# Optimization experiments

Hardware: AMD Instinct MI355X
Metric: run time of the kernel (lower is better)

## Reference

```python
import jax, jax.numpy as jnp
import numpy as np

SINK_MAX = 128  # max materialized sink tokens (atten_sink counts are < 64)
NEG_INF = -1e30


def _gather_paged(kv, block_table, pos):
    """Gather tokens from a paged KV cache.
    kv: [num_blocks, block_size, 2, Hkv, D]; block_table: [B, max_blocks] int;
    pos: [B, L] token positions (assumed clipped to valid range).
    Returns [B, L, 2, Hkv, D]."""
    nb, bs = kv.shape[0], kv.shape[1]
    B = pos.shape[0]
    blk = jnp.take_along_axis(block_table, pos // bs, axis=1)  # [B, L]
    flat_idx = blk * bs + pos % bs                              # [B, L]
    kv_flat = kv.reshape(nb * bs, *kv.shape[2:])
    return kv_flat[flat_idx]


def setup_inputs() -> dict:
    key = jax.random.key(0)
    ks = jax.random.split(key, 6)
    B, H, Hkv, D = 32, 32, 4, 128
    NB, BS, NBC = 2048, 128, 512
    MAX_BLK, MAX_CBLK, NSEL = 64, 16, 256
    query = jax.random.normal(ks[0], (B, H, D), dtype=jnp.float32)
    ori_kv = jax.random.normal(ks[1], (NB, BS, 2, Hkv, D), dtype=jnp.float32)
    cmp_kv = jax.random.normal(ks[2], (NBC, BS, 2, Hkv, D), dtype=jnp.float32)
    ori_block_table = (jnp.arange(B * MAX_BLK) % NB).reshape(B, MAX_BLK).astype(jnp.int32)
    cmp_block_table = (jnp.arange(B * MAX_CBLK) % NBC).reshape(B, MAX_CBLK).astype(jnp.int32)
    atten_sink = jax.random.randint(ks[3], (B,), 1, 64, dtype=jnp.int32)
    seqused_kv = jax.random.randint(ks[4], (B,), 4096, 8192, dtype=jnp.int32)
    cmp_sparse_indices = jnp.sort(jax.random.randint(ks[5], (B, NSEL), 0, 1024, dtype=jnp.int32), axis=1)
    return {
        'query_npu': query,
        'q_act_seqs_npu': jnp.ones((B,), dtype=jnp.int32),
        'ori_kv_npu': ori_kv,
        'cmp_kv_npu': cmp_kv,
        'ori_block_table_npu': ori_block_table,
        'cmp_block_table_npu': cmp_block_table,
        'atten_sink_npu': atten_sink,
        'seqused_kv_npu': seqused_kv,
        'cmp_sparse_indices_npu': cmp_sparse_indices,
        'softmax_scale': float(1.0 / np.sqrt(D)),
        'win_size': 512,
        'cmp_ratio': 4,
    }


def reference(query_npu, q_act_seqs_npu, ori_kv_npu, cmp_kv_npu,
              ori_block_table_npu, cmp_block_table_npu, atten_sink_npu,
              seqused_kv_npu, cmp_sparse_indices_npu, softmax_scale,
              win_size, cmp_ratio):
    B, H, D = query_npu.shape
    Hkv = ori_kv_npu.shape[3]
    G = H // Hkv
    bs = ori_kv_npu.shape[1]
    seq = seqused_kv_npu[:, None].astype(jnp.int32)          # [B,1]
    sink = atten_sink_npu[:, None].astype(jnp.int32)         # [B,1]

    # --- sink tokens (first atten_sink tokens of the original cache) ---
    pos_s = jnp.broadcast_to(jnp.arange(SINK_MAX, dtype=jnp.int32)[None, :], (B, SINK_MAX))
    mask_s = (pos_s < sink) & (pos_s < seq)
    kv_s = _gather_paged(ori_kv_npu, ori_block_table_npu, jnp.clip(pos_s, 0))

    # --- sliding window (last win_size original tokens, excluding sink overlap) ---
    pos_w = seq - win_size + jnp.arange(win_size, dtype=jnp.int32)[None, :]
    mask_w = (pos_w >= 0) & (pos_w >= sink)
    kv_w = _gather_paged(ori_kv_npu, ori_block_table_npu, jnp.clip(pos_w, 0))

    # --- sparse-selected compressed tokens ---
    cmp_len = seq // cmp_ratio
    idx_c = cmp_sparse_indices_npu.astype(jnp.int32)         # [B, NSEL]
    mask_c = idx_c < cmp_len
    kv_c = _gather_paged(cmp_kv_npu, cmp_block_table_npu, jnp.clip(idx_c, 0))

    # --- combine all KV sources: [B, L, 2, Hkv, D] ---
    kv = jnp.concatenate([kv_s, kv_w, kv_c], axis=1)
    k, v = kv[:, :, 0], kv[:, :, 1]                           # [B, L, Hkv, D]
    mask = jnp.concatenate([mask_s, mask_w, mask_c], axis=1)  # [B, L]

    # --- GQA attention: heads grouped per kv head ---
    q = query_npu.reshape(B, Hkv, G, D)
    logits = jnp.einsum('bkgd,blkd->bkgl', q, k) * softmax_scale
    logits = jnp.where(mask[:, None, None, :], logits, NEG_INF)
    p = jax.nn.softmax(logits, axis=-1)
    out = jnp.einsum('bkgl,blkd->bkgd', p, v)
    return out.reshape(B, H, D)
```

## Files before the change

kernel.cpp:

```cpp
#include <hip/hip_runtime.h>

constexpr int B_    = 32;
constexpr int H_    = 32;
constexpr int HKV_  = 4;
constexpr int G_    = 8;
constexpr int D_    = 128;
constexpr int BS_   = 128;
constexpr int MAXBLK_  = 64;
constexpr int MAXCBLK_ = 16;
constexpr int NSEL_    = 256;
constexpr int SINKMAX_ = 128;
constexpr int WIN_     = 512;
constexpr int P_       = 8;
constexpr float MSHIFT = 24.0f;

__global__ __launch_bounds__(256, 4) void sfa_partial_kernel(
    const float* __restrict__ q,
    const float* __restrict__ ori_kv,
    const float* __restrict__ cmp_kv,
    const int*   __restrict__ ori_bt,
    const int*   __restrict__ cmp_bt,
    const int*   __restrict__ sinkp,
    const int*   __restrict__ seqp,
    const int*   __restrict__ selp,
    const float* __restrict__ scalep,
    const int*   __restrict__ ratiop,
    float* __restrict__ o_out,
    float* __restrict__ s_out)
{
  const int part = blockIdx.x;
  const int kh   = blockIdx.y;
  const int b    = blockIdx.z;
  const int tid  = threadIdx.x;
  const int grp  = tid >> 5;
  const int j    = tid & 31;
  const int wave = tid >> 6;
  const int h    = ((j & 1) << 2) | (j & 2) | ((j >> 2) & 1);

  const float scale = scalep[0];
  const int ratio   = ratiop[0];
  const int seq     = seqp[b];
  const int sink    = sinkp[b];
  const int cmp_len = seq / ratio;

  const int sbt0 = ori_bt[b * MAXBLK_];
  int wbase = seq - WIN_; if (wbase < 0) wbase = 0;
  const int w0 = wbase >> 7;
  auto obt = [&](int k) { int w = w0 + k; if (w > MAXBLK_ - 1) w = MAXBLK_ - 1;
                          return ori_bt[b * MAXBLK_ + w]; };
  const int wb0 = obt(0), wb1 = obt(1), wb2 = obt(2), wb3 = obt(3), wb4 = obt(4);
  const int cb0 = cmp_bt[b * MAXCBLK_ + 0], cb1 = cmp_bt[b * MAXCBLK_ + 1];
  const int cb2 = cmp_bt[b * MAXCBLK_ + 2], cb3 = cmp_bt[b * MAXCBLK_ + 3];
  const int cb4 = cmp_bt[b * MAXCBLK_ + 4], cb5 = cmp_bt[b * MAXCBLK_ + 5];
  const int cb6 = cmp_bt[b * MAXCBLK_ + 6], cb7 = cmp_bt[b * MAXCBLK_ + 7];

  float4 qf[G_];
  const float* qb = q + ((size_t)b * H_ + (size_t)kh * G_) * D_ + 4 * j;
#pragma unroll
  for (int g = 0; g < G_; ++g) qf[g] = *(const float4*)(qb + g * D_);

  float  s_acc = 0.f;
  float4 oacc[G_];
#pragma unroll
  for (int m = 0; m < G_; ++m) oacc[m] = make_float4(0.f, 0.f, 0.f, 0.f);

  int s_end = sink; if (s_end < 0) s_end = 0; if (s_end > SINKMAX_) s_end = SINKMAX_;
  const int sB0 = s_end;
  const int sC0 = s_end + WIN_;
  const int L   = s_end + WIN_ + NSEL_;
  const int chunk = (L + P_ - 1) / P_;
  const int lo = part * chunk;
  int hi = lo + chunk; if (hi > L) hi = L;

  auto process = [&](const float4 kf, const float4 vf, const float msk) {
    float lg[G_];
#pragma unroll
    for (int g = 0; g < G_; ++g)
      lg[g] = qf[g].x * kf.x + qf[g].y * kf.y + qf[g].z * kf.z + qf[g].w * kf.w;
    const bool p0 = j & 1, p1 = j & 2, p2 = j & 4;
    float s4[4];
#pragma unroll
    for (int i4 = 0; i4 < 4; ++i4) {
      const float keep = p0 ? lg[4 + i4] : lg[i4];
      const float send = p0 ? lg[i4]     : lg[4 + i4];
      s4[i4] = keep + __shfl_xor(send, 1, 64);
    }
    float s2[2];
#pragma unroll
    for (int i2 = 0; i2 < 2; ++i2) {
      const float keep = p1 ? s4[2 + i2] : s4[i2];
      const float send = p1 ? s4[i2]     : s4[2 + i2];
      s2[i2] = keep + __shfl_xor(send, 2, 64);
    }
    const float keep = p2 ? s2[1] : s2[0];
    const float send = p2 ? s2[0] : s2[1];
    float v1 = keep + __shfl_xor(send, 4, 64);
    v1 += __shfl_xor(v1, 8, 64);
    v1 += __shfl_xor(v1, 16, 64);
    const float e = __expf(fminf(fmaf(v1, scale, -MSHIFT), 80.f)) * msk;
    s_acc += e;
    const float g2a = e,   g2b = __shfl_xor(e, 4, 64);
    const float g4a = g2a, g4b = g2b;
    const float g4c = __shfl_xor(g2a, 2, 64), g4d = __shfl_xor(g2b, 2, 64);
    const float pm0 = g4a, pm1 = g4b, pm2 = g4c, pm3 = g4d;
    const float pm4 = __shfl_xor(g4a, 1, 64), pm5 = __shfl_xor(g4b, 1, 64);
    const float pm6 = __shfl_xor(g4c, 1, 64), pm7 = __shfl_xor(g4d, 1, 64);
    oacc[0].x += pm0 * vf.x; oacc[0].y += pm0 * vf.y; oacc[0].z += pm0 * vf.z; oacc[0].w += pm0 * vf.w;
    oacc[1].x += pm1 * vf.x; oacc[1].y += pm1 * vf.y; oacc[1].z += pm1 * vf.z; oacc[1].w += pm1 * vf.w;
    oacc[2].x += pm2 * vf.x; oacc[2].y += pm2 * vf.y; oacc[2].z += pm2 * vf.z; oacc[2].w += pm2 * vf.w;
    oacc[3].x += pm3 * vf.x; oacc[3].y += pm3 * vf.y; oacc[3].z += pm3 * vf.z; oacc[3].w += pm3 * vf.w;
    oacc[4].x += pm4 * vf.x; oacc[4].y += pm4 * vf.y; oacc[4].z += pm4 * vf.z; oacc[4].w += pm4 * vf.w;
    oacc[5].x += pm5 * vf.x; oacc[5].y += pm5 * vf.y; oacc[5].z += pm5 * vf.z; oacc[5].w += pm5 * vf.w;
    oacc[6].x += pm6 * vf.x; oacc[6].y += pm6 * vf.y; oacc[6].z += pm6 * vf.z; oacc[6].w += pm6 * vf.w;
    oacc[7].x += pm7 * vf.x; oacc[7].y += pm7 * vf.y; oacc[7].z += pm7 * vf.z; oacc[7].w += pm7 * vf.w;
  };

#define SEG_LOOP(S0X, S1X, ADDR_CODE)                                          \
  {                                                                            \
    const int s0q = (S0X), s1q = (S1X);                                        \
    int iq = s0q + ((lo + grp - s0q) & 7);                                     \
    if (iq < s1q) {                                                            \
      const float* kbC; float mC;                                              \
      { const int ti = iq; const float* akb; float amsk; ADDR_CODE;            \
        kbC = akb; mC = amsk; }                                                \
      float4 kfC = *(const float4*)(kbC + 4 * j);                              \
      float4 vfC = *(const float4*)(kbC + HKV_ * D_ + 4 * j);                  \
      for (; iq < s1q; iq += 8) {                                              \
        int inq = iq + 8; if (inq >= s1q) inq = s1q - 1;                       \
        const float* kbN; float mN;                                            \
        { const int ti = inq; const float* akb; float amsk; ADDR_CODE;         \
          kbN = akb; mN = amsk; }                                              \
        const float4 kfN = *(const float4*)(kbN + 4 * j);                      \
        const float4 vfN = *(const float4*)(kbN + HKV_ * D_ + 4 * j);          \
        process(kfC, vfC, mC);                                                 \
        kfC = kfN; vfC = vfN; mC = mN;                                         \
      }                                                                        \
    }                                                                          \
  }

  SEG_LOOP(lo, (hi < sB0 ? hi : sB0), {
    amsk = (ti < seq) ? 1.f : 0.f;
    akb = ori_kv + (((size_t)(sbt0 * BS_ + ti)) << 10) + kh * D_;
  });

  SEG_LOOP((lo > sB0 ? lo : sB0), (hi < sC0 ? hi : sC0), {
    const int pos = seq - WIN_ + (ti - sB0);
    amsk = (pos >= 0 && pos >= sink) ? 1.f : 0.f;
    const int pc = pos > 0 ? pos : 0;
    const int wi = (pc >> 7) - w0;
    int blk = wb0;
    blk = (wi == 1) ? wb1 : blk; blk = (wi == 2) ? wb2 : blk;
    blk = (wi == 3) ? wb3 : blk; blk = (wi == 4) ? wb4 : blk;
    akb = ori_kv + (((size_t)(blk * BS_ + (pc & (BS_ - 1)))) << 10) + kh * D_;
  });

  SEG_LOOP((lo > sC0 ? lo : sC0), hi, {
    const int idx = selp[b * NSEL_ + (ti - sC0)];
    amsk = (idx < cmp_len) ? 1.f : 0.f;
    const int pc = idx > 0 ? idx : 0;
    const int ci = pc >> 7;
    int blk = cb0;
    blk = (ci == 1) ? cb1 : blk; blk = (ci == 2) ? cb2 : blk;
    blk = (ci == 3) ? cb3 : blk; blk = (ci == 4) ? cb4 : blk;
    blk = (ci == 5) ? cb5 : blk; blk = (ci == 6) ? cb6 : blk;
    blk = (ci == 7) ? cb7 : blk;
    akb = cmp_kv + (((size_t)(blk * BS_ + (pc & (BS_ - 1)))) << 10) + kh * D_;
  });
#undef SEG_LOOP

  s_acc += __shfl_xor(s_acc, 32, 64);
  float* of = reinterpret_cast<float*>(oacc);
#pragma unroll
  for (int t = 0; t < 32; ++t) of[t] += __shfl_xor(of[t], 32, 64);

  __shared__ float lds_o[4][G_][D_];
  __shared__ float lds_s[4][G_];
  if ((tid & 63) < 32) {
#pragma unroll
    for (int m = 0; m < G_; ++m)
      *(float4*)&lds_o[wave][h ^ m][4 * j] = oacc[m];
    if (j < 8) lds_s[wave][h] = s_acc;
  }
  __syncthreads();

#pragma unroll
  for (int e = tid; e < G_ * D_; e += 256) {
    const int g = e >> 7, d = e & (D_ - 1);
    const float num = lds_o[0][g][d] + lds_o[1][g][d] + lds_o[2][g][d] + lds_o[3][g][d];
    o_out[(((size_t)(b * HKV_ + kh) * P_ + part) * G_ + g) * D_ + d] = num;
  }
  if (tid < G_) {
    s_out[((size_t)(b * HKV_ + kh) * P_ + part) * G_ + tid] =
        lds_s[0][tid] + lds_s[1][tid] + lds_s[2][tid] + lds_s[3][tid];
  }
}

__global__ __launch_bounds__(256) void sfa_combine_kernel(
    const float* __restrict__ op, const float* __restrict__ sp,
    float* __restrict__ out)
{
  const int idx = blockIdx.x * 256 + threadIdx.x;
  const int d  = idx & (D_ - 1);
  const int hh = (idx >> 7) & (H_ - 1);
  const int b  = idx >> 12;
  const int kh = hh >> 3, g = hh & 7;
  float num = 0.f, den = 0.f;
#pragma unroll
  for (int p = 0; p < P_; ++p) {
    num += op[(((size_t)(b * HKV_ + kh) * P_ + p) * G_ + g) * D_ + d];
    den += sp[((size_t)(b * HKV_ + kh) * P_ + p) * G_ + g];
  }
  out[idx] = num / den;
}

extern "C" void kernel_launch(void* const* d_in, const int* in_sizes, int n_in,
                              void* d_out, int out_size, void* d_ws, size_t ws_size,
                              hipStream_t stream) {
  const float* q      = (const float*)d_in[0];
  const float* ori_kv = (const float*)d_in[2];
  const float* cmp_kv = (const float*)d_in[3];
  const int*   ori_bt = (const int*)d_in[4];
  const int*   cmp_bt = (const int*)d_in[5];
  const int*   sinkp  = (const int*)d_in[6];
  const int*   seqp   = (const int*)d_in[7];
  const int*   selp   = (const int*)d_in[8];
  const float* scalep = (const float*)d_in[9];
  const int*   ratiop = (const int*)d_in[11];
  float* out = (float*)d_out;

  float* op = (float*)d_ws;
  float* sp = op + (size_t)P_ * B_ * HKV_ * G_ * D_;

  sfa_partial_kernel<<<dim3(P_, HKV_, B_), 256, 0, stream>>>(
      q, ori_kv, cmp_kv, ori_bt, cmp_bt, sinkp, seqp, selp, scalep, ratiop,
      op, sp);
  sfa_combine_kernel<<<(B_ * H_ * D_) / 256, 256, 0, stream>>>(op, sp, out);
}
```

Measured before the change: 27.63 us.

## Stream KV rows into LDS with async global_load_lds and a 4-deep pipeline

Replaces the three per-segment register-prefetch loops with one unified loop over the partition. K/V rows are issued through global_load_lds into a per-wave 4-stage LDS ring, with manual vmcnt waits. Masks are precomputed into a bitmask, and the selected indices are preloaded into lanes and fetched by shuffle. The aim is more memory requests in flight to hide gather latency, at the cost of branchy unified address math, LDS round trips, and reliance on exact vmcnt accounting.

Result: slower. 72.02 us (+160.6%).

```diff
diff --git a/kernel.cpp b/kernel.cpp
--- a/kernel.cpp
+++ b/kernel.cpp
@@ -1,4 +1,5 @@
 #include <hip/hip_runtime.h>
+#include <stdint.h>
 
 constexpr int B_    = 32;
 constexpr int H_    = 32;
@@ -12,7 +13,14 @@
 constexpr int SINKMAX_ = 128;
 constexpr int WIN_     = 512;
 constexpr int P_       = 8;
+constexpr int DP_      = 4;
 constexpr float MSHIFT = 24.0f;
+
+__device__ __forceinline__ void gload_lds16(const float* src, float* dst) {
+  __builtin_amdgcn_global_load_lds(
+      (__attribute__((address_space(1))) void*)(const_cast<float*>(src)),
+      (__attribute__((address_space(3))) void*)(dst), 16, 0, 0);
+}
 
 __global__ __launch_bounds__(256, 4) void sfa_partial_kernel(
     const float* __restrict__ q,
@@ -28,6 +36,9 @@
     float* __restrict__ o_out,
     float* __restrict__ s_out)
 {
+  __shared__ float smem[4 * DP_ * 512];
+  __shared__ float lds_s[4][G_];
+
   const int part = blockIdx.x;
   const int kh   = blockIdx.y;
   const int b    = blockIdx.z;
@@ -35,6 +46,7 @@
   const int grp  = tid >> 5;
   const int j    = tid & 31;
   const int wave = tid >> 6;
+  const int lane = tid & 63;
   const int h    = ((j & 1) << 2) | (j & 2) | ((j >> 2) & 1);
 
   const float scale = scalep[0];
@@ -54,16 +66,6 @@
   const int cb4 = cmp_bt[b * MAXCBLK_ + 4], cb5 = cmp_bt[b * MAXCBLK_ + 5];
   const int cb6 = cmp_bt[b * MAXCBLK_ + 6], cb7 = cmp_bt[b * MAXCBLK_ + 7];
 
-  float4 qf[G_];
-  const float* qb = q + ((size_t)b * H_ + (size_t)kh * G_) * D_ + 4 * j;
-#pragma unroll
-  for (int g = 0; g < G_; ++g) qf[g] = *(const float4*)(qb + g * D_);
-
-  float  s_acc = 0.f;
-  float4 oacc[G_];
-#pragma unroll
-  for (int m = 0; m < G_; ++m) oacc[m] = make_float4(0.f, 0.f, 0.f, 0.f);
-
   int s_end = sink; if (s_end < 0) s_end = 0; if (s_end > SINKMAX_) s_end = SINKMAX_;
   const int sB0 = s_end;
   const int sC0 = s_end + WIN_;
@@ -71,6 +73,64 @@
   const int chunk = (L + P_ - 1) / P_;
   const int lo = part * chunk;
   int hi = lo + chunk; if (hi > L) hi = L;
+  const int n_iter = (hi - lo + 7) >> 3;
+  const int cf = sC0 + (((lo + grp) - sC0) & 7);
+
+  const int sel_l = selp[b * NSEL_ + (cf - sC0) + 8 * j];
+  float4 qf[G_];
+  const float* qb = q + ((size_t)b * H_ + (size_t)kh * G_) * D_ + 4 * j;
+#pragma unroll
+  for (int g = 0; g < G_; ++g) qf[g] = *(const float4*)(qb + g * D_);
+
+  float  s_acc = 0.f;
+  float4 oacc[G_];
+#pragma unroll
+  for (int m = 0; m < G_; ++m) oacc[m] = make_float4(0.f, 0.f, 0.f, 0.f);
+
+  unsigned mbits = 0;
+  for (int t = 0; t < n_iter; ++t) {
+    const int ti  = lo + grp + (t << 3);
+    const int tcl = ti < hi ? ti : hi - 1;
+    const bool inC = tcl >= sC0;
+    const bool inB = (!inC) && (tcl >= sB0);
+    const int posB = tcl + (seq - WIN_ - sB0);
+    int mI = (tcl - cf) >> 3; mI = mI < 0 ? 0 : (mI > 31 ? 31 : mI);
+    const int idx = __shfl(sel_l, mI, 32);
+    const bool ok = inC ? (idx < cmp_len)
+                  : inB ? (posB >= 0 && posB >= sink)
+                        : (tcl < seq);
+    if (ti < hi && ok) mbits |= (1u << t);
+  }
+
+  auto issue = [&](int t) {
+    const int ti  = lo + grp + (t << 3);
+    const int tcl = ti < hi ? ti : hi - 1;
+    const bool inC = tcl >= sC0;
+    const bool inB = (!inC) && (tcl >= sB0);
+    const int posB = tcl + (seq - WIN_ - sB0);
+    const int pcB = posB > 0 ? posB : 0;
+    const int wi = (pcB >> 7) - w0;
+    int blkB = wb0;
+    blkB = (wi == 1) ? wb1 : blkB; blkB = (wi == 2) ? wb2 : blkB;
+    blkB = (wi == 3) ? wb3 : blkB; blkB = (wi == 4) ? wb4 : blkB;
+    int mI = (tcl - cf) >> 3; mI = mI < 0 ? 0 : (mI > 31 ? 31 : mI);
+    const int idx = __shfl(sel_l, mI, 32);
+    const int pcC = idx > 0 ? idx : 0;
+    const int ci = pcC >> 7;
+    int blkC = cb0;
+    blkC = (ci == 1) ? cb1 : blkC; blkC = (ci == 2) ? cb2 : blkC;
+    blkC = (ci == 3) ? cb3 : blkC; blkC = (ci == 4) ? cb4 : blkC;
+    blkC = (ci == 5) ? cb5 : blkC; blkC = (ci == 6) ? cb6 : blkC;
+    blkC = (ci == 7) ? cb7 : blkC;
+    const int row = inC ? (blkC * BS_ + (pcC & (BS_ - 1)))
+                  : inB ? (blkB * BS_ + (pcB & (BS_ - 1)))
+                        : (sbt0 * BS_ + tcl);
+    const float* bp = inC ? cmp_kv : ori_kv;
+    const float* src = bp + (((size_t)row) << 10) + kh * D_ + 4 * j;
+    float* dstK = &smem[wave * (DP_ * 512) + (t & (DP_ - 1)) * 512];
+    gload_lds16(src, dstK);
+    gload_lds16(src + 512, dstK + 256);
+  };
 
   auto process = [&](const float4 kf, const float4 vf, const float msk) {
     float lg[G_];
@@ -115,67 +175,48 @@
     oacc[7].x += pm7 * vf.x; oacc[7].y += pm7 * vf.y; oacc[7].z += pm7 * vf.z; oacc[7].w += pm7 * vf.w;
   };
 
-#define SEG_LOOP(S0X, S1X, ADDR_CODE)                                          \
-  {                                                                            \
-    const int s0q = (S0X), s1q = (S1X);                                        \
-    int iq = s0q + ((lo + grp - s0q) & 7);                                     \
-    if (iq < s1q) {                                                            \
-      const float* kbC; float mC;                                              \
-      { const int ti = iq; const float* akb; float amsk; ADDR_CODE;            \
-        kbC = akb; mC = amsk; }                                                \
-      float4 kfC = *(const float4*)(kbC + 4 * j);                              \
-      float4 vfC = *(const float4*)(kbC + HKV_ * D_ + 4 * j);                  \
-      for (; iq < s1q; iq += 8) {                                              \
-        int inq = iq + 8; if (inq >= s1q) inq = s1q - 1;                       \
-        const float* kbN; float mN;                                            \
-        { const int ti = inq; const float* akb; float amsk; ADDR_CODE;         \
-          kbN = akb; mN = amsk; }                                              \
-        const float4 kfN = *(const float4*)(kbN + 4 * j);                      \
-        const float4 vfN = *(const float4*)(kbN + HKV_ * D_ + 4 * j);          \
-        process(kfC, vfC, mC);                                                 \
-        kfC = kfN; vfC = vfN; mC = mN;                                         \
-      }                                                                        \
-    }                                                                          \
-  }
-
-  SEG_LOOP(lo, (hi < sB0 ? hi : sB0), {
-    amsk = (ti < seq) ? 1.f : 0.f;
-    akb = ori_kv + (((size_t)(sbt0 * BS_ + ti)) << 10) + kh * D_;
-  });
-
-  SEG_LOOP((lo > sB0 ? lo : sB0), (hi < sC0 ? hi : sC0), {
-    const int pos = seq - WIN_ + (ti - sB0);
-    amsk = (pos >= 0 && pos >= sink) ? 1.f : 0.f;
-    const int pc = pos > 0 ? pos : 0;
-    const int wi = (pc >> 7) - w0;
-    int blk = wb0;
-    blk = (wi == 1) ? wb1 : blk; blk = (wi == 2) ? wb2 : blk;
-    blk = (wi == 3) ? wb3 : blk; blk = (wi == 4) ? wb4 : blk;
-    akb = ori_kv + (((size_t)(blk * BS_ + (pc & (BS_ - 1)))) << 10) + kh * D_;
-  });
-
-  SEG_LOOP((lo > sC0 ? lo : sC0), hi, {
-    const int idx = selp[b * NSEL_ + (ti - sC0)];
-    amsk = (idx < cmp_len) ? 1.f : 0.f;
-    const int pc = idx > 0 ? idx : 0;
-    const int ci = pc >> 7;
-    int blk = cb0;
-    blk = (ci == 1) ? cb1 : blk; blk = (ci == 2) ? cb2 : blk;
-    blk = (ci == 3) ? cb3 : blk; blk = (ci == 4) ? cb4 : blk;
-    blk = (ci == 5) ? cb5 : blk; blk = (ci == 6) ? cb6 : blk;
-    blk = (ci == 7) ? cb7 : blk;
-    akb = cmp_kv + (((size_t)(blk * BS_ + (pc & (BS_ - 1)))) << 10) + kh * D_;
-  });
-#undef SEG_LOOP
+  auto consume = [&](int t) {
+    const float* sb = &smem[wave * (DP_ * 512) + (t & (DP_ - 1)) * 512];
+    const float4 kf = *(const float4*)(sb + 4 * lane);
+    const float4 vf = *(const float4*)(sb + 256 + 4 * lane);
+    const float msk = ((mbits >> t) & 1u) ? 1.f : 0.f;
+    process(kf, vf, msk);
+  };
+
+  asm volatile("s_waitcnt vmcnt(0)" ::: "memory");
+
+  if (n_iter >= DP_) {
+    issue(0); issue(1); issue(2);
+    for (int t = 0; t < n_iter; ++t) {
+      const int tn = t + DP_ - 1;
+      if (tn < n_iter) {
+        issue(tn);
+        asm volatile("s_waitcnt vmcnt(6)" ::: "memory");
+      } else if (tn == n_iter) {
+        asm volatile("s_waitcnt vmcnt(4)" ::: "memory");
+      } else if (tn == n_iter + 1) {
+        asm volatile("s_waitcnt vmcnt(2)" ::: "memory");
+      } else {
+        asm volatile("s_waitcnt vmcnt(0)" ::: "memory");
+      }
+      consume(t);
+    }
+  } else {
+    for (int t = 0; t < n_iter; ++t) {
+      issue(t);
+      asm volatile("s_waitcnt vmcnt(0)" ::: "memory");
+      consume(t);
+    }
+  }
 
   s_acc += __shfl_xor(s_acc, 32, 64);
   float* of = reinterpret_cast<float*>(oacc);
 #pragma unroll
   for (int t = 0; t < 32; ++t) of[t] += __shfl_xor(of[t], 32, 64);
 
-  __shared__ float lds_o[4][G_][D_];
-  __shared__ float lds_s[4][G_];
-  if ((tid & 63) < 32) {
+  __syncthreads();
+  float (*lds_o)[G_][D_] = (float(*)[G_][D_])smem;
+  if (lane < 32) {
 #pragma unroll
     for (int m = 0; m < G_; ++m)
       *(float4*)&lds_o[wave][h ^ m][4 * j] = oacc[m];
```

## Merge KV heads into 1024-thread blocks and shuffle-broadcast sparse indices

Applied to the files above, without the earlier changes.

Each block now covers all four KV heads of a batch partition with 1024 threads (16 waves), so the grid shrinks from P×HKV×B to P×B. Sparse indices are loaded once per lane up front and fetched through a warp shuffle instead of a global load per token. The cross-wave reduction becomes a two-stage LDS add before the store. This is meant to cut index-load latency and per-block setup, but it lowers block count (256 blocks), may raise register pressure under the larger launch bound, and adds an extra barrier.

Result: slower. 28.30 us (+2.4%).

```diff
diff --git a/kernel.cpp b/kernel.cpp
--- a/kernel.cpp
+++ b/kernel.cpp
@@ -14,7 +14,7 @@
 constexpr int P_       = 8;
 constexpr float MSHIFT = 24.0f;
 
-__global__ __launch_bounds__(256, 4) void sfa_partial_kernel(
+__global__ __launch_bounds__(1024, 4) void sfa_partial_kernel(
     const float* __restrict__ q,
     const float* __restrict__ ori_kv,
     const float* __restrict__ cmp_kv,
@@ -29,12 +29,15 @@
     float* __restrict__ s_out)
 {
   const int part = blockIdx.x;
-  const int kh   = blockIdx.y;
-  const int b    = blockIdx.z;
+  const int b    = blockIdx.y;
   const int tid  = threadIdx.x;
-  const int grp  = tid >> 5;
+  const int wave = tid >> 6;
+  const int kh   = wave >> 2;
+  const int wq   = wave & 3;
+  const int gi   = (tid >> 5) & 1;
+  const int qg   = wq * 2 + gi;
   const int j    = tid & 31;
-  const int wave = tid >> 6;
+  const int lane = tid & 63;
   const int h    = ((j & 1) << 2) | (j & 2) | ((j >> 2) & 1);
 
   const float scale = scalep[0];
@@ -71,6 +74,8 @@
   const int chunk = (L + P_ - 1) / P_;
   const int lo = part * chunk;
   int hi = lo + chunk; if (hi > L) hi = L;
+  const int cf = sC0 + (((lo + qg) - sC0) & 7);
+  const int sel_l = selp[b * NSEL_ + (cf - sC0) + 8 * j];
 
   auto process = [&](const float4 kf, const float4 vf, const float msk) {
     float lg[G_];
@@ -118,7 +123,7 @@
 #define SEG_LOOP(S0X, S1X, ADDR_CODE)                                          \
   {                                                                            \
     const int s0q = (S0X), s1q = (S1X);                                        \
-    int iq = s0q + ((lo + grp - s0q) & 7);                                     \
+    int iq = s0q + ((lo + qg - s0q) & 7);                                      \
     if (iq < s1q) {                                                            \
       const float* kbC; float mC;                                              \
       { const int ti = iq; const float* akb; float amsk; ADDR_CODE;            \
@@ -155,7 +160,8 @@
   });
 
   SEG_LOOP((lo > sC0 ? lo : sC0), hi, {
-    const int idx = selp[b * NSEL_ + (ti - sC0)];
+    int mI = (ti - cf) >> 3; mI = mI < 0 ? 0 : (mI > 31 ? 31 : mI);
+    const int idx = __shfl(sel_l, mI, 32);
     amsk = (idx < cmp_len) ? 1.f : 0.f;
     const int pc = idx > 0 ? idx : 0;
     const int ci = pc >> 7;
@@ -173,25 +179,38 @@
 #pragma unroll
   for (int t = 0; t < 32; ++t) of[t] += __shfl_xor(of[t], 32, 64);
 
-  __shared__ float lds_o[4][G_][D_];
-  __shared__ float lds_s[4][G_];
-  if ((tid & 63) < 32) {
+  __shared__ float lds_o[HKV_][2][G_][D_];
+  __shared__ float lds_s[HKV_][2][G_];
+  if (wq >= 2 && lane < 32) {
 #pragma unroll
     for (int m = 0; m < G_; ++m)
-      *(float4*)&lds_o[wave][h ^ m][4 * j] = oacc[m];
-    if (j < 8) lds_s[wave][h] = s_acc;
+      *(float4*)&lds_o[kh][wq - 2][h ^ m][4 * j] = oacc[m];
+    if (j < 8) lds_s[kh][wq - 2][h] = s_acc;
   }
   __syncthreads();
-
-#pragma unroll
-  for (int e = tid; e < G_ * D_; e += 256) {
-    const int g = e >> 7, d = e & (D_ - 1);
-    const float num = lds_o[0][g][d] + lds_o[1][g][d] + lds_o[2][g][d] + lds_o[3][g][d];
-    o_out[(((size_t)(b * HKV_ + kh) * P_ + part) * G_ + g) * D_ + d] = num;
-  }
-  if (tid < G_) {
-    s_out[((size_t)(b * HKV_ + kh) * P_ + part) * G_ + tid] =
-        lds_s[0][tid] + lds_s[1][tid] + lds_s[2][tid] + lds_s[3][tid];
+  if (wq < 2 && lane < 32) {
+#pragma unroll
+    for (int m = 0; m < G_; ++m) {
+      float4 p = *(float4*)&lds_o[kh][wq][h ^ m][4 * j];
+      p.x += oacc[m].x; p.y += oacc[m].y; p.z += oacc[m].z; p.w += oacc[m].w;
+      *(float4*)&lds_o[kh][wq][h ^ m][4 * j] = p;
+    }
+    if (j < 8) lds_s[kh][wq][h] += s_acc;
+  }
+  __syncthreads();
+
+#pragma unroll
+  for (int e = tid; e < HKV_ * G_ * D_; e += 1024) {
+    const int kk = e >> 10;
+    const int g  = (e >> 7) & 7;
+    const int d  = e & (D_ - 1);
+    const float num = lds_o[kk][0][g][d] + lds_o[kk][1][g][d];
+    o_out[(((size_t)(b * HKV_ + kk) * P_ + part) * G_ + g) * D_ + d] = num;
+  }
+  if (tid < HKV_ * G_) {
+    const int kk = tid >> 3, g = tid & 7;
+    s_out[((size_t)(b * HKV_ + kk) * P_ + part) * G_ + g] =
+        lds_s[kk][0][g] + lds_s[kk][1][g];
   }
 }
 
@@ -231,7 +250,7 @@
   float* op = (float*)d_ws;
   float* sp = op + (size_t)P_ * B_ * HKV_ * G_ * D_;
 
-  sfa_partial_kernel<<<dim3(P_, HKV_, B_), 256, 0, stream>>>(
+  sfa_partial_kernel<<<dim3(P_, B_), 1024, 0, stream>>>(
       q, ori_kv, cmp_kv, ori_bt, cmp_bt, sinkp, seqp, selp, scalep, ratiop,
       op, sp);
   sfa_combine_kernel<<<(B_ * H_ * D_) / 256, 256, 0, stream>>>(op, sp, out);
```

## Split attention into score pass and PV pass with LDS-staged probabilities and DPP reductions

Applied to the files above, without the earlier changes.

Restructures the per-token loop into two passes. The first loads K, computes logits with DPP and ds_swizzle cross-lane reductions instead of __shfl_xor, and writes exp scores to LDS. After a barrier, the second pass loads V and accumulates PV using the scores read back from LDS, which removes the permutation shuffles used to distribute probabilities. Both passes unroll by two tokens with deeper prefetch, and the sparse-index loads are gathered up front with one load per lane and broadcast by shuffle. The cost is an extra barrier, LDS traffic, and recomputing addresses twice, plus a risk of exceeding the LMAX_ bound on tokens per group.

Measured after the change: 28.99 us. 1.05x slower.

```diff
diff --git a/kernel.cpp b/kernel.cpp
--- a/kernel.cpp
+++ b/kernel.cpp
@@ -12,7 +12,22 @@
 constexpr int SINKMAX_ = 128;
 constexpr int WIN_     = 512;
 constexpr int P_       = 8;
+constexpr int LMAX_    = 16;
 constexpr float MSHIFT = 24.0f;
+
+template <int CTRL>
+__device__ __forceinline__ float dpp_mov(float x) {
+  return __int_as_float(__builtin_amdgcn_update_dpp(
+      0, __float_as_int(x), CTRL, 0xF, 0xF, true));
+}
+constexpr int DPP_XOR1 = 0xB1;
+constexpr int DPP_XOR2 = 0x4E;
+constexpr int DPP_XOR8 = 0x128;
+template <int PATT>
+__device__ __forceinline__ float swz_add(float x) {
+  return x + __int_as_float(
+      __builtin_amdgcn_ds_swizzle(__float_as_int(x), PATT));
+}
 
 __global__ __launch_bounds__(256, 4) void sfa_partial_kernel(
     const float* __restrict__ q,
@@ -28,6 +43,10 @@
     float* __restrict__ o_out,
     float* __restrict__ s_out)
 {
+  __shared__ float e_lds[8][LMAX_][G_];
+  __shared__ float lds_o[4][G_][D_];
+  __shared__ float lds_s[4][G_];
+
   const int part = blockIdx.x;
   const int kh   = blockIdx.y;
   const int b    = blockIdx.z;
@@ -35,7 +54,9 @@
   const int grp  = tid >> 5;
   const int j    = tid & 31;
   const int wave = tid >> 6;
-  const int h    = ((j & 1) << 2) | (j & 2) | ((j >> 2) & 1);
+  const int lane = tid & 63;
+  const int h    = ((j & 1) << 2) | (j & 2) | ((j >> 3) & 1);
+  const bool wr8 = ((j & 20) == 0);
 
   const float scale = scalep[0];
   const int ratio   = ratiop[0];
@@ -54,16 +75,6 @@
   const int cb4 = cmp_bt[b * MAXCBLK_ + 4], cb5 = cmp_bt[b * MAXCBLK_ + 5];
   const int cb6 = cmp_bt[b * MAXCBLK_ + 6], cb7 = cmp_bt[b * MAXCBLK_ + 7];
 
-  float4 qf[G_];
-  const float* qb = q + ((size_t)b * H_ + (size_t)kh * G_) * D_ + 4 * j;
-#pragma unroll
-  for (int g = 0; g < G_; ++g) qf[g] = *(const float4*)(qb + g * D_);
-
-  float  s_acc = 0.f;
-  float4 oacc[G_];
-#pragma unroll
-  for (int m = 0; m < G_; ++m) oacc[m] = make_float4(0.f, 0.f, 0.f, 0.f);
-
   int s_end = sink; if (s_end < 0) s_end = 0; if (s_end > SINKMAX_) s_end = SINKMAX_;
   const int sB0 = s_end;
   const int sC0 = s_end + WIN_;
@@ -71,115 +82,171 @@
   const int chunk = (L + P_ - 1) / P_;
   const int lo = part * chunk;
   int hi = lo + chunk; if (hi > L) hi = L;
-
-  auto process = [&](const float4 kf, const float4 vf, const float msk) {
+  const int cf = sC0 + (((lo + grp) - sC0) & 7);
+  const int sel_l = selp[b * NSEL_ + (cf - sC0) + 8 * j];
+
+  float4 qf[G_];
+  {
+    const float* qb = q + ((size_t)b * H_ + (size_t)kh * G_) * D_ + 4 * j;
+#pragma unroll
+    for (int g = 0; g < G_; ++g) qf[g] = *(const float4*)(qb + g * D_);
+  }
+
+  float s_acc = 0.f;
+
+  auto pass1_tok = [&](const float4 kf, const float msk, const int l) {
     float lg[G_];
 #pragma unroll
     for (int g = 0; g < G_; ++g)
       lg[g] = qf[g].x * kf.x + qf[g].y * kf.y + qf[g].z * kf.z + qf[g].w * kf.w;
-    const bool p0 = j & 1, p1 = j & 2, p2 = j & 4;
+    const bool p0 = j & 1, p1 = j & 2, p3 = j & 8;
     float s4[4];
 #pragma unroll
     for (int i4 = 0; i4 < 4; ++i4) {
       const float keep = p0 ? lg[4 + i4] : lg[i4];
       const float send = p0 ? lg[i4]     : lg[4 + i4];
-      s4[i4] = keep + __shfl_xor(send, 1, 64);
+      s4[i4] = keep + dpp_mov<DPP_XOR1>(send);
     }
     float s2[2];
 #pragma unroll
     for (int i2 = 0; i2 < 2; ++i2) {
       const float keep = p1 ? s4[2 + i2] : s4[i2];
       const float send = p1 ? s4[i2]     : s4[2 + i2];
-      s2[i2] = keep + __shfl_xor(send, 2, 64);
+      s2[i2] = keep + dpp_mov<DPP_XOR2>(send);
     }
-    const float keep = p2 ? s2[1] : s2[0];
-    const float send = p2 ? s2[0] : s2[1];
-    float v1 = keep + __shfl_xor(send, 4, 64);
-    v1 += __shfl_xor(v1, 8, 64);
-    v1 += __shfl_xor(v1, 16, 64);
+    const float keep = p3 ? s2[1] : s2[0];
+    const float send = p3 ? s2[0] : s2[1];
+    float v1 = keep + dpp_mov<DPP_XOR8>(send);
+    v1 = swz_add<0x101F>(v1);
+    v1 = swz_add<0x401F>(v1);
     const float e = __expf(fminf(fmaf(v1, scale, -MSHIFT), 80.f)) * msk;
     s_acc += e;
-    const float g2a = e,   g2b = __shfl_xor(e, 4, 64);
-    const float g4a = g2a, g4b = g2b;
-    const float g4c = __shfl_xor(g2a, 2, 64), g4d = __shfl_xor(g2b, 2, 64);
-    const float pm0 = g4a, pm1 = g4b, pm2 = g4c, pm3 = g4d;
-    const float pm4 = __shfl_xor(g4a, 1, 64), pm5 = __shfl_xor(g4b, 1, 64);
-    const float pm6 = __shfl_xor(g4c, 1, 64), pm7 = __shfl_xor(g4d, 1, 64);
-    oacc[0].x += pm0 * vf.x; oacc[0].y += pm0 * vf.y; oacc[0].z += pm0 * vf.z; oacc[0].w += pm0 * vf.w;
-    oacc[1].x += pm1 * vf.x; oacc[1].y += pm1 * vf.y; oacc[1].z += pm1 * vf.z; oacc[1].w += pm1 * vf.w;
-    oacc[2].x += pm2 * vf.x; oacc[2].y += pm2 * vf.y; oacc[2].z += pm2 * vf.z; oacc[2].w += pm2 * vf.w;
-    oacc[3].x += pm3 * vf.x; oacc[3].y += pm3 * vf.y; oacc[3].z += pm3 * vf.z; oacc[3].w += pm3 * vf.w;
-    oacc[4].x += pm4 * vf.x; oacc[4].y += pm4 * vf.y; oacc[4].z += pm4 * vf.z; oacc[4].w += pm4 * vf.w;
-    oacc[5].x += pm5 * vf.x; oacc[5].y += pm5 * vf.y; oacc[5].z += pm5 * vf.z; oacc[5].w += pm5 * vf.w;
-    oacc[6].x += pm6 * vf.x; oacc[6].y += pm6 * vf.y; oacc[6].z += pm6 * vf.z; oacc[6].w += pm6 * vf.w;
-    oacc[7].x += pm7 * vf.x; oacc[7].y += pm7 * vf.y; oacc[7].z += pm7 * vf.z; oacc[7].w += pm7 * vf.w;
+    if (wr8) e_lds[grp][l][h] = e;
   };
 
-#define SEG_LOOP(S0X, S1X, ADDR_CODE)                                          \
+#define P1_LOOP(S0X, S1X, ADDR_CODE)                                           \
   {                                                                            \
     const int s0q = (S0X), s1q = (S1X);                                        \
     int iq = s0q + ((lo + grp - s0q) & 7);                                     \
     if (iq < s1q) {                                                            \
-      const float* kbC; float mC;                                              \
-      { const int ti = iq; const float* akb; float amsk; ADDR_CODE;            \
-        kbC = akb; mC = amsk; }                                                \
-      float4 kfC = *(const float4*)(kbC + 4 * j);                              \
-      float4 vfC = *(const float4*)(kbC + HKV_ * D_ + 4 * j);                  \
-      for (; iq < s1q; iq += 8) {                                              \
-        int inq = iq + 8; if (inq >= s1q) inq = s1q - 1;                       \
-        const float* kbN; float mN;                                            \
-        { const int ti = inq; const float* akb; float amsk; ADDR_CODE;         \
-          kbN = akb; mN = amsk; }                                              \
-        const float4 kfN = *(const float4*)(kbN + 4 * j);                      \
-        const float4 vfN = *(const float4*)(kbN + HKV_ * D_ + 4 * j);          \
-        process(kfC, vfC, mC);                                                 \
-        kfC = kfN; vfC = vfN; mC = mN;                                         \
+      const float *pA, *pB; float mA, mB;                                      \
+      { const int tic = iq; const float* akb; float amsk; ADDR_CODE;           \
+        pA = akb; mA = amsk; }                                                 \
+      { int t2 = iq + 8; const int tic = t2 < s1q ? t2 : s1q - 1;              \
+        const float* akb; float amsk; ADDR_CODE;                               \
+        pB = akb; mB = (iq + 8 < s1q) ? amsk : 0.f; }                          \
+      float4 kA = *(const float4*)(pA + 4 * j);                                \
+      float4 kB = *(const float4*)(pB + 4 * j);                                \
+      for (; iq < s1q; iq += 16) {                                             \
+        const float *pN, *pN2; float mN, mN2;                                  \
+        { int t2 = iq + 16; const int tic = t2 < s1q ? t2 : s1q - 1;           \
+          const float* akb; float amsk; ADDR_CODE;                             \
+          pN = akb; mN = (iq + 16 < s1q) ? amsk : 0.f; }                       \
+        { int t2 = iq + 24; const int tic = t2 < s1q ? t2 : s1q - 1;           \
+          const float* akb; float amsk; ADDR_CODE;                             \
+          pN2 = akb; mN2 = (iq + 24 < s1q) ? amsk : 0.f; }                     \
+        pass1_tok(kA, mA, (iq - lo) >> 3);                                     \
+        kA = *(const float4*)(pN + 4 * j);                                     \
+        pass1_tok(kB, mB, (iq + 8 - lo) >> 3);                                 \
+        kB = *(const float4*)(pN2 + 4 * j);                                    \
+        mA = mN; mB = mN2;                                                     \
       }                                                                        \
     }                                                                          \
   }
 
-  SEG_LOOP(lo, (hi < sB0 ? hi : sB0), {
-    amsk = (ti < seq) ? 1.f : 0.f;
-    akb = ori_kv + (((size_t)(sbt0 * BS_ + ti)) << 10) + kh * D_;
-  });
-
-  SEG_LOOP((lo > sB0 ? lo : sB0), (hi < sC0 ? hi : sC0), {
-    const int pos = seq - WIN_ + (ti - sB0);
-    amsk = (pos >= 0 && pos >= sink) ? 1.f : 0.f;
-    const int pc = pos > 0 ? pos : 0;
-    const int wi = (pc >> 7) - w0;
-    int blk = wb0;
-    blk = (wi == 1) ? wb1 : blk; blk = (wi == 2) ? wb2 : blk;
-    blk = (wi == 3) ? wb3 : blk; blk = (wi == 4) ? wb4 : blk;
-    akb = ori_kv + (((size_t)(blk * BS_ + (pc & (BS_ - 1)))) << 10) + kh * D_;
-  });
-
-  SEG_LOOP((lo > sC0 ? lo : sC0), hi, {
-    const int idx = selp[b * NSEL_ + (ti - sC0)];
-    amsk = (idx < cmp_len) ? 1.f : 0.f;
-    const int pc = idx > 0 ? idx : 0;
-    const int ci = pc >> 7;
-    int blk = cb0;
-    blk = (ci == 1) ? cb1 : blk; blk = (ci == 2) ? cb2 : blk;
-    blk = (ci == 3) ? cb3 : blk; blk = (ci == 4) ? cb4 : blk;
-    blk = (ci == 5) ? cb5 : blk; blk = (ci == 6) ? cb6 : blk;
-    blk = (ci == 7) ? cb7 : blk;
-    akb = cmp_kv + (((size_t)(blk * BS_ + (pc & (BS_ - 1)))) << 10) + kh * D_;
-  });
-#undef SEG_LOOP
+#define ADDR_A {                                                               \
+    amsk = (tic < seq) ? 1.f : 0.f;                                            \
+    akb = ori_kv + (((size_t)(sbt0 * BS_ + tic)) << 10) + kh * D_; }
+#define ADDR_B {                                                               \
+    const int pos = tic + (seq - WIN_ - sB0);                                  \
+    amsk = (pos >= 0 && pos >= sink) ? 1.f : 0.f;                              \
+    const int pc = pos > 0 ? pos : 0;                                          \
+    const int wi = (pc >> 7) - w0;                                             \
+    int blk = wb0;                                                             \
+    blk = (wi == 1) ? wb1 : blk; blk = (wi == 2) ? wb2 : blk;                  \
+    blk = (wi == 3) ? wb3 : blk; blk = (wi == 4) ? wb4 : blk;                  \
+    akb = ori_kv + (((size_t)(blk * BS_ + (pc & (BS_ - 1)))) << 10) + kh * D_; }
+#define ADDR_C {                                                               \
+    int mI = (tic - cf) >> 3; mI = mI < 0 ? 0 : (mI > 31 ? 31 : mI);           \
+    const int idx = __shfl(sel_l, mI, 32);                                     \
+    amsk = (idx < cmp_len) ? 1.f : 0.f;                                        \
+    const int pc = idx > 0 ? idx : 0;                                          \
+    const int ci = pc >> 7;                                                    \
+    int blk = cb0;                                                             \
+    blk = (ci == 1) ? cb1 : blk; blk = (ci == 2) ? cb2 : blk;                  \
+    blk = (ci == 3) ? cb3 : blk; blk = (ci == 4) ? cb4 : blk;                  \
+    blk = (ci == 5) ? cb5 : blk; blk = (ci == 6) ? cb6 : blk;                  \
+    blk = (ci == 7) ? cb7 : blk;                                               \
+    akb = cmp_kv + (((size_t)(blk * BS_ + (pc & (BS_ - 1)))) << 10) + kh * D_; }
+
+  P1_LOOP(lo, (hi < sB0 ? hi : sB0), ADDR_A);
+  P1_LOOP((lo > sB0 ? lo : sB0), (hi < sC0 ? hi : sC0), ADDR_B);
+  P1_LOOP((lo > sC0 ? lo : sC0), hi, ADDR_C);
+#undef P1_LOOP
+
+  __syncthreads();
+
+  float4 oacc[G_];
+#pragma unroll
+  for (int m = 0; m < G_; ++m) oacc[m] = make_float4(0.f, 0.f, 0.f, 0.f);
+
+  auto pass2_tok = [&](const float4 vf, const int l) {
+    const float4 e03 = *(const float4*)&e_lds[grp][l][0];
+    const float4 e47 = *(const float4*)&e_lds[grp][l][4];
+    oacc[0].x += e03.x * vf.x; oacc[0].y += e03.x * vf.y; oacc[0].z += e03.x * vf.z; oacc[0].w += e03.x * vf.w;
+    oacc[1].x += e03.y * vf.x; oacc[1].y += e03.y * vf.y; oacc[1].z += e03.y * vf.z; oacc[1].w += e03.y * vf.w;
+    oacc[2].x += e03.z * vf.x; oacc[2].y += e03.z * vf.y; oacc[2].z += e03.z * vf.z; oacc[2].w += e03.z * vf.w;
+    oacc[3].x += e03.w * vf.x; oacc[3].y += e03.w * vf.y; oacc[3].z += e03.w * vf.z; oacc[3].w += e03.w * vf.w;
+    oacc[4].x += e47.x * vf.x; oacc[4].y += e47.x * vf.y; oacc[4].z += e47.x * vf.z; oacc[4].w += e47.x * vf.w;
+    oacc[5].x += e47.y * vf.x; oacc[5].y += e47.y * vf.y; oacc[5].z += e47.y * vf.z; oacc[5].w += e47.y * vf.w;
+    oacc[6].x += e47.z * vf.x; oacc[6].y += e47.z * vf.y; oacc[6].z += e47.z * vf.z; oacc[6].w += e47.z * vf.w;
+    oacc[7].x += e47.w * vf.x; oacc[7].y += e47.w * vf.y; oacc[7].z += e47.w * vf.z; oacc[7].w += e47.w * vf.w;
+  };
+
+#define P2_LOOP(S0X, S1X, ADDR_CODE)                                           \
+  {                                                                            \
+    const int s0q = (S0X), s1q = (S1X);                                        \
+    int iq = s0q + ((lo + grp - s0q) & 7);                                     \
+    if (iq < s1q) {                                                            \
+      const float *pA, *pB;                                                    \
+      { const int tic = iq; const float* akb; float amsk; ADDR_CODE;           \
+        (void)amsk; pA = akb; }                                                \
+      { int t2 = iq + 8; const int tic = t2 < s1q ? t2 : s1q - 1;              \
+        const float* akb; float amsk; ADDR_CODE; (void)amsk; pB = akb; }       \
+      float4 vA = *(const float4*)(pA + HKV_ * D_ + 4 * j);                    \
+      float4 vB = *(const float4*)(pB + HKV_ * D_ + 4 * j);                    \
+      for (; iq < s1q; iq += 16) {                                             \
+        const float *pN, *pN2;                                                 \
+        { int t2 = iq + 16; const int tic = t2 < s1q ? t2 : s1q - 1;           \
+          const float* akb; float amsk; ADDR_CODE; (void)amsk; pN = akb; }     \
+        { int t2 = iq + 24; const int tic = t2 < s1q ? t2 : s1q - 1;           \
+          const float* akb; float amsk; ADDR_CODE; (void)amsk; pN2 = akb; }    \
+        pass2_tok(vA, (iq - lo) >> 3);                                         \
+        vA = *(const float4*)(pN + HKV_ * D_ + 4 * j);                         \
+        if (iq + 8 < s1q) pass2_tok(vB, (iq + 8 - lo) >> 3);                   \
+        vB = *(const float4*)(pN2 + HKV_ * D_ + 4 * j);                        \
+      }                                                                        \
+    }                                                                          \
+  }
+
+  P2_LOOP(lo, (hi < sB0 ? hi : sB0), ADDR_A);
+  P2_LOOP((lo > sB0 ? lo : sB0), (hi < sC0 ? hi : sC0), ADDR_B);
+  P2_LOOP((lo > sC0 ? lo : sC0), hi, ADDR_C);
+#undef P2_LOOP
+#undef ADDR_A
+#undef ADDR_B
+#undef ADDR_C
 
   s_acc += __shfl_xor(s_acc, 32, 64);
   float* of = reinterpret_cast<float*>(oacc);
 #pragma unroll
   for (int t = 0; t < 32; ++t) of[t] += __shfl_xor(of[t], 32, 64);
 
-  __shared__ float lds_o[4][G_][D_];
-  __shared__ float lds_s[4][G_];
-  if ((tid & 63) < 32) {
+  if (lane < 32) {
 #pragma unroll
     for (int m = 0; m < G_; ++m)
-      *(float4*)&lds_o[wave][h ^ m][4 * j] = oacc[m];
-    if (j < 8) lds_s[wave][h] = s_acc;
+      *(float4*)&lds_o[wave][m][4 * j] = oacc[m];
+    if (wr8) lds_s[wave][h] = s_acc;
   }
   __syncthreads();
 
```
